# Optimization experiments

Hardware: AMD Instinct MI355X
Metric: run time of the kernel (lower is better)

Reference implementation:

```python
import jax, jax.numpy as jnp
import numpy as np
import math

NH, NKV, HD = 8, 1, 128
SOFTCAP = 30.0
ROPE_BASE = 500000.0


def _rope_tables(T, hd, base):
    half = hd // 2
    inv_freq = 1.0 / (base ** (np.arange(half, dtype=np.float32) / half))
    t = np.arange(T, dtype=np.float32)
    ang = np.outer(t, inv_freq)  # [T, half]
    return jnp.asarray(np.cos(ang)), jnp.asarray(np.sin(ang))


def apply_rope(x, cos, sin):
    # x: [B, T, H, hd]; cos/sin: [T, hd//2]
    half = x.shape[-1] // 2
    x1, x2 = x[..., :half], x[..., half:]
    T = x.shape[1]
    c = cos[:T][None, :, None, :]
    s = sin[:T][None, :, None, :]
    return jnp.concatenate([x1 * c - x2 * s, x1 * s + x2 * c], axis=-1)


def setup_inputs() -> dict:
    key = jax.random.key(0)
    ks = jax.random.split(key, 5)
    B, T, D = 4, 2048, 1024
    KD = NKV * HD
    x = jax.random.normal(ks[0], (B, T, D), dtype=jnp.float32)
    Wq = jax.random.normal(ks[1], (D, D), dtype=jnp.float32) * (D ** -0.5)
    Wk = jax.random.normal(ks[2], (KD, D), dtype=jnp.float32) * (D ** -0.5)
    Wv = jax.random.normal(ks[3], (KD, D), dtype=jnp.float32) * (D ** -0.5)
    Wo = jax.random.normal(ks[4], (D, D), dtype=jnp.float32) * (D ** -0.5)
    qk_gain = jnp.full((NH,), 1.5, dtype=jnp.float32)  # qk_gain_init
    cos, sin = _rope_tables(T, HD, ROPE_BASE)
    return {"x": x, "Wq": Wq, "Wk": Wk, "Wv": Wv, "Wo": Wo,
            "qk_gain": qk_gain, "cos": cos, "sin": sin}


def reference(x, Wq, Wk, Wv, Wo, qk_gain, cos, sin):
    B, T, D = x.shape
    # projections (QuantLinear with qat disabled == plain linear, no bias)
    q = (x @ Wq.T).reshape(B, T, NH, HD)
    k = (x @ Wk.T).reshape(B, T, NKV, HD)
    v = (x @ Wv.T).reshape(B, T, NKV, HD)
    q = apply_rope(q, cos, sin)
    k = apply_rope(k, cos, sin)
    # learned per-head QK gain applied to queries
    q = q * qk_gain[None, None, :, 1 - 1][..., None] if False else q * qk_gain[None, None, :, None]
    # GQA: broadcast the single kv head across NH query heads
    scale = 1.0 / math.sqrt(HD)
    scores = jnp.einsum('bqhd,bkgd->bhqk', q, k) * scale  # g==NKV==1 broadcast
    # logit softcap before masking/softmax
    scores = SOFTCAP * jnp.tanh(scores / SOFTCAP)
    causal = jnp.tril(jnp.ones((T, T), dtype=bool))
    scores = jnp.where(causal[None, None], scores, -jnp.inf)
    attn = jax.nn.softmax(scores, axis=-1)  # [B, NH, T, T]
    out = jnp.einsum('bhqk,bkgd->bqhd', attn, v).reshape(B, T, NH * HD)
    return out @ Wo.T
```

## Files before the change

### kernel.cpp

```cpp
#include <hip/hip_runtime.h>
#include <hip/hip_bf16.h>

#define B_ 4
#define T_ 2048
#define D_ 1024
#define NH_ 8
#define HD_ 128

typedef short short8 __attribute__((ext_vector_type(8)));
typedef float floatx4 __attribute__((ext_vector_type(4)));

#if __has_builtin(__builtin_amdgcn_exp2f)
#define EXP2F __builtin_amdgcn_exp2f
#else
#define EXP2F exp2f
#endif
#if __has_builtin(__builtin_amdgcn_rcpf)
#define RCPF __builtin_amdgcn_rcpf
#else
__device__ __forceinline__ float RCPF(float x) { return 1.f / x; }
#endif

#if __has_builtin(__builtin_amdgcn_global_load_lds)
#define G2L(gp, lp)                                                        \
  __builtin_amdgcn_global_load_lds(                                        \
      (const __attribute__((address_space(1))) unsigned int*)(gp),         \
      (__attribute__((address_space(3))) unsigned int*)(lp), 16, 0, 0)
#else
#define G2L(gp, lp) (*(uint4*)(lp) = *(const uint4*)(gp))
#endif

__device__ __forceinline__ unsigned short f2b(float f) {
  union { float fl; unsigned int i; } v; v.fl = f;
  unsigned int r = v.i + 0x7fffu + ((v.i >> 16) & 1u);
  return (unsigned short)(r >> 16);
}
__device__ __forceinline__ unsigned int pack_bf16(float a, float b) {
  unsigned int ua = __float_as_uint(a) + 0x8000u;
  unsigned int ub = __float_as_uint(b) + 0x8000u;
  return (ua >> 16) | (ub & 0xffff0000u);
}

__global__ __launch_bounds__(256) void cvt_kernel(
    const float* __restrict__ x,  const float* __restrict__ wq,
    const float* __restrict__ wk, const float* __restrict__ wv,
    const float* __restrict__ wo, unsigned short* __restrict__ dst)
{
  size_t i = ((size_t)blockIdx.x * 256 + threadIdx.x) * 8;
  const float* src; size_t off;
  if      (i <  8388608u) { src = x;  off = i; }
  else if (i <  9437184u) { src = wq; off = i - 8388608u; }
  else if (i <  9568256u) { src = wk; off = i - 9437184u; }
  else if (i <  9699328u) { src = wv; off = i - 9568256u; }
  else                    { src = wo; off = i - 9699328u; }
  float4 a = *(const float4*)(src + off);
  float4 b = *(const float4*)(src + off + 4);
  uint4 o;
  o.x = pack_bf16(a.x, a.y); o.y = pack_bf16(a.z, a.w);
  o.z = pack_bf16(b.x, b.y); o.w = pack_bf16(b.z, b.w);
  *(uint4*)(dst + i) = o;
}

template <bool C_F32>
__device__ __forceinline__ void gemm_body_1024(
    const unsigned short* __restrict__ Arow0,
    const unsigned short* __restrict__ Btile,
    void* __restrict__ Cb, int ldC)
{
  __shared__ unsigned short As[128 * 32];
  __shared__ unsigned short Bs[128 * 32];
  const int tid = threadIdx.x;
  const int lane = tid & 63;
  const int w = tid >> 6;
  const int wr = w >> 1, wc = w & 1;
  const int l15 = lane & 15, quad = lane >> 4;

  const unsigned short* a_src = Arow0 + (size_t)(tid >> 2) * 1024 + (tid & 3) * 8;
  const unsigned short* b_src = Btile + (size_t)(tid >> 2) * 1024 + (tid & 3) * 8;
  unsigned short* a_dst = &As[(tid >> 2) * 32 + (tid & 3) * 8];
  unsigned short* b_dst = &Bs[(tid >> 2) * 32 + (tid & 3) * 8];

  floatx4 zero = {0.f, 0.f, 0.f, 0.f};
  floatx4 acc[4][4];
#pragma unroll
  for (int i = 0; i < 4; i++)
#pragma unroll
    for (int j = 0; j < 4; j++) acc[i][j] = zero;

  for (int k0 = 0; k0 < 1024; k0 += 32) {
    __syncthreads();
    G2L(a_src + k0,         a_dst);
    G2L(a_src + 65536 + k0, a_dst + 2048);
    G2L(b_src + k0,         b_dst);
    G2L(b_src + 65536 + k0, b_dst + 2048);
    __syncthreads();
    short8 af[4], bfr[4];
#pragma unroll
    for (int i = 0; i < 4; i++)
      af[i] = *(const short8*)&As[(wr * 64 + i * 16 + l15) * 32 + quad * 8];
#pragma unroll
    for (int j = 0; j < 4; j++)
      bfr[j] = *(const short8*)&Bs[(wc * 64 + j * 16 + l15) * 32 + quad * 8];
#pragma unroll
    for (int i = 0; i < 4; i++)
#pragma unroll
      for (int j = 0; j < 4; j++)
        acc[i][j] = __builtin_amdgcn_mfma_f32_16x16x32_bf16(af[i], bfr[j], acc[i][j], 0, 0, 0);
  }
#pragma unroll
  for (int i = 0; i < 4; i++)
#pragma unroll
    for (int j = 0; j < 4; j++)
#pragma unroll
      for (int r = 0; r < 4; r++) {
        size_t off = (size_t)(wr * 64 + i * 16 + quad * 4 + r) * ldC + wc * 64 + j * 16 + l15;
        if (C_F32) ((float*)Cb)[off] = acc[i][j][r];
        else ((unsigned short*)Cb)[off] = f2b(acc[i][j][r]);
      }
}

__global__ __launch_bounds__(256) void gemm_qkv_kernel(
    const unsigned short* __restrict__ x,
    const unsigned short* __restrict__ Wq,
    const unsigned short* __restrict__ Wk,
    const unsigned short* __restrict__ Wv,
    unsigned short* __restrict__ q,
    unsigned short* __restrict__ k,
    unsigned short* __restrict__ v)
{
  const int bx = blockIdx.x, by = blockIdx.y;
  const unsigned short* Btile;
  unsigned short* C;
  int ldC, col0;
  if (by < 8) { Btile = Wq + (size_t)by * 128 * 1024; C = q; ldC = 1024; col0 = by * 128; }
  else if (by == 8) { Btile = Wk; C = k; ldC = 128; col0 = 0; }
  else { Btile = Wv; C = v; ldC = 128; col0 = 0; }
  gemm_body_1024<false>(x + (size_t)bx * 128 * 1024, Btile,
                        C + (size_t)bx * 128 * ldC + col0, ldC);
}

__global__ __launch_bounds__(256) void gemm_out_kernel(
    const unsigned short* __restrict__ ao,
    const unsigned short* __restrict__ Wo,
    float* __restrict__ out)
{
  const int bx = blockIdx.x, by = blockIdx.y;
  gemm_body_1024<true>(ao + (size_t)bx * 128 * 1024, Wo + (size_t)by * 128 * 1024,
                       out + (size_t)bx * 128 * 1024 + by * 128, 1024);
}

__global__ __launch_bounds__(256) void rope_kernel(
    unsigned short* __restrict__ q,
    unsigned short* __restrict__ k,
    const float* __restrict__ cosT,
    const float* __restrict__ sinT,
    const float* __restrict__ gain)
{
  const int NQ = B_ * T_ * NH_ * 64;
  int idx = blockIdx.x * 256 + threadIdx.x;
  if (idx < NQ) {
    int i = idx & 63, h = (idx >> 6) & 7, bt = idx >> 9, t = bt & (T_ - 1);
    float c = cosT[t * 64 + i], s = sinT[t * 64 + i];
    float g = gain[h] * 0.0029462782549439484f;
    size_t base = (size_t)bt * 1024 + h * 128;
    float x1 = __bfloat162float(*(const __hip_bfloat16*)&q[base + i]);
    float x2 = __bfloat162float(*(const __hip_bfloat16*)&q[base + 64 + i]);
    q[base + i]      = f2b((x1 * c - x2 * s) * g);
    q[base + 64 + i] = f2b((x1 * s + x2 * c) * g);
  } else if (idx < NQ + B_ * T_ * 64) {
    int j = idx - NQ;
    int i = j & 63, bt = j >> 6, t = bt & (T_ - 1);
    float c = cosT[t * 64 + i], s = sinT[t * 64 + i];
    size_t base = (size_t)bt * 128;
    float x1 = __bfloat162float(*(const __hip_bfloat16*)&k[base + i]);
    float x2 = __bfloat162float(*(const __hip_bfloat16*)&k[base + 64 + i]);
    k[base + i]      = f2b(x1 * c - x2 * s);
    k[base + 64 + i] = f2b(x1 * s + x2 * c);
  }
}

__global__ __launch_bounds__(256) void vtrans_kernel(
    const unsigned short* __restrict__ v,
    unsigned short* __restrict__ vT)
{
  __shared__ unsigned short tile[32 * 136];
  const int b = blockIdx.y, t0 = blockIdx.x * 32, tid = threadIdx.x;
  for (int u = tid; u < 512; u += 256) {
    int r = u >> 4, c = u & 15;
    *(uint4*)&tile[r * 136 + c * 8] =
        *(const uint4*)(v + ((size_t)(b * T_ + t0 + r)) * 128 + c * 8);
  }
  __syncthreads();
  for (int u = tid; u < 512; u += 256) {
    int d = u >> 2, c = u & 3;
    short8 val;
#pragma unroll
    for (int j = 0; j < 8; j++) val[j] = (short)tile[(c * 8 + j) * 136 + d];
    *(short8*)(vT + ((size_t)(b * 128 + d)) * T_ + t0 + c * 8) = val;
  }
}

__global__ __launch_bounds__(256) void attn_kernel(
    const unsigned short* __restrict__ q,
    const unsigned short* __restrict__ k,
    const unsigned short* __restrict__ vT,
    unsigned short* __restrict__ ao)
{
  __shared__ unsigned short Ks[16 * 264];
  __shared__ unsigned short Vts[128 * 40];
  __shared__ unsigned short Pw[4][32 * 40];

  const int pr = blockIdx.x, h = blockIdx.y, b = blockIdx.z;
  const int tid = threadIdx.x, lane = tid & 63, w = tid >> 6;
  const int l15 = lane & 15, quad = lane >> 4;

  const unsigned short* ksrc =
      k + (size_t)b * T_ * 128 + (size_t)(tid >> 4) * 128 + (tid & 15) * 8;
  unsigned short* kdst0 = &Ks[(tid & 15) * 264 + (tid >> 4) * 8];
  unsigned short* kdst1 = kdst0 + 16 * 8;
  const unsigned short* vsrc =
      vT + (size_t)b * 128 * T_ + (size_t)(tid >> 2) * T_ + (tid & 3) * 8;
  unsigned short* vdst0 = &Vts[(tid >> 2) * 40 + (tid & 3) * 8];
  unsigned short* vdst1 = vdst0 + 64 * 40;

  const floatx4 zero = {0.f, 0.f, 0.f, 0.f};

  for (int pass = 0; pass < 2; pass++) {
    const int qblock = pass ? (15 - pr) : pr;
    const int qbase = qblock * 128;
    const int qw = qbase + w * 32;
    const int nkt = qblock * 4 + 4;

    short8 qf[2][4];
#pragma unroll
    for (int g = 0; g < 2; g++) {
      const unsigned short* qrow =
          q + ((size_t)(b * T_ + qw + g * 16 + l15) * NH_ + h) * HD_;
#pragma unroll
      for (int c = 0; c < 4; c++) qf[g][c] = *(const short8*)(qrow + c * 32 + quad * 8);
    }

    float l_i[2] = {0.f, 0.f};
    floatx4 acc[8][2];
#pragma unroll
    for (int d = 0; d < 8; d++) { acc[d][0] = zero; acc[d][1] = zero; }

    uint4 kr0 = *(const uint4*)(ksrc);
    uint4 kr1 = *(const uint4*)(ksrc + 2048);
    uint4 vr0 = *(const uint4*)(vsrc);
    uint4 vr1 = *(const uint4*)(vsrc + (size_t)64 * T_);

    for (int kt = 0; kt < nkt; kt++) {
      __syncthreads();
      *(uint4*)kdst0 = kr0; *(uint4*)kdst1 = kr1;
      *(uint4*)vdst0 = vr0; *(uint4*)vdst1 = vr1;
      int ktn = (kt + 1 < nkt) ? kt + 1 : kt;
      kr0 = *(const uint4*)(ksrc + (size_t)ktn * 4096);
      kr1 = *(const uint4*)(ksrc + (size_t)ktn * 4096 + 2048);
      vr0 = *(const uint4*)(vsrc + ktn * 32);
      vr1 = *(const uint4*)(vsrc + (size_t)64 * T_ + ktn * 32);
      __syncthreads();

      if (kt * 32 <= qw + 31) {
        floatx4 st[2][2] = {{zero, zero}, {zero, zero}};
#pragma unroll
        for (int c = 0; c < 4; c++) {
          const int dg = (c * 4 + quad) * 264;
          short8 kf0 = *(const short8*)&Ks[dg + l15 * 8];
          short8 kf1 = *(const short8*)&Ks[dg + (16 + l15) * 8];
          st[0][0] = __builtin_amdgcn_mfma_f32_16x16x32_bf16(kf0, qf[0][c], st[0][0], 0, 0, 0);
          st[0][1] = __builtin_amdgcn_mfma_f32_16x16x32_bf16(kf0, qf[1][c], st[0][1], 0, 0, 0);
          st[1][0] = __builtin_amdgcn_mfma_f32_16x16x32_bf16(kf1, qf[0][c], st[1][0], 0, 0, 0);
          st[1][1] = __builtin_amdgcn_mfma_f32_16x16x32_bf16(kf1, qf[1][c], st[1][1], 0, 0, 0);
        }
        float rs[2] = {0.f, 0.f};
#pragma unroll
        for (int f = 0; f < 2; f++)
#pragma unroll
          for (int g = 0; g < 2; g++) {
            float pv[4];
            const int qrow = qw + g * 16 + l15;
#pragma unroll
            for (int r = 0; r < 4; r++) {
              float s = st[f][g][r];
              float e = EXP2F(2.8853901f * s);
              float u = RCPF(e + 1.f);
              float p = EXP2F(-86.561707f * u);
              int key = kt * 32 + f * 16 + quad * 4 + r;
              p = (key <= qrow) ? p : 0.f;
              pv[r] = p;
              rs[g] += p;
            }
            uint2 pk;
            pk.x = pack_bf16(pv[0], pv[1]);
            pk.y = pack_bf16(pv[2], pv[3]);
            *(uint2*)&Pw[w][(g * 16 + l15) * 40 + f * 16 + quad * 4] = pk;
          }
#pragma unroll
        for (int g = 0; g < 2; g++) {
          float r2 = rs[g] + __shfl_xor(rs[g], 16);
          l_i[g] += r2 + __shfl_xor(r2, 32);
        }
        asm volatile("s_waitcnt lgkmcnt(0)" ::: "memory");
        short8 pf0 = *(const short8*)&Pw[w][l15 * 40 + quad * 8];
        short8 pf1 = *(const short8*)&Pw[w][(16 + l15) * 40 + quad * 8];
#pragma unroll
        for (int d = 0; d < 8; d++) {
          short8 vf = *(const short8*)&Vts[(d * 16 + l15) * 40 + quad * 8];
          acc[d][0] = __builtin_amdgcn_mfma_f32_16x16x32_bf16(vf, pf0, acc[d][0], 0, 0, 0);
          acc[d][1] = __builtin_amdgcn_mfma_f32_16x16x32_bf16(vf, pf1, acc[d][1], 0, 0, 0);
        }
      }
    }

#pragma unroll
    for (int g = 0; g < 2; g++) {
      float linv = 1.f / l_i[g];
      unsigned short* aop =
          ao + ((size_t)(b * T_ + qw + g * 16 + l15) * NH_ + h) * HD_ + quad * 4;
#pragma unroll
      for (int d = 0; d < 8; d++) {
        uint2 o;
        o.x = pack_bf16(acc[d][g][0] * linv, acc[d][g][1] * linv);
        o.y = pack_bf16(acc[d][g][2] * linv, acc[d][g][3] * linv);
        *(uint2*)(aop + d * 16) = o;
      }
    }
  }
}

extern "C" void kernel_launch(void* const* d_in, const int* in_sizes, int n_in,
                              void* d_out, int out_size, void* d_ws, size_t ws_size,
                              hipStream_t stream) {
  const float* x    = (const float*)d_in[0];
  const float* Wq   = (const float*)d_in[1];
  const float* Wk   = (const float*)d_in[2];
  const float* Wv   = (const float*)d_in[3];
  const float* Wo   = (const float*)d_in[4];
  const float* gain = (const float*)d_in[5];
  const float* cosT = (const float*)d_in[6];
  const float* sinT = (const float*)d_in[7];
  float* out = (float*)d_out;

  unsigned short* ws = (unsigned short*)d_ws;
  unsigned short* blob = ws;
  unsigned short* xb  = blob;
  unsigned short* Wqb = blob + 8388608u;
  unsigned short* Wkb = blob + 9437184u;
  unsigned short* Wvb = blob + 9568256u;
  unsigned short* Wob = blob + 9699328u;
  unsigned short* q   = ws + 10747904u;
  unsigned short* kk  = ws + 19136512u;
  unsigned short* v   = ws + 20185088u;
  unsigned short* vT  = ws + 21233664u;
  unsigned short* ao  = xb;

  cvt_kernel<<<5248, 256, 0, stream>>>(x, Wq, Wk, Wv, Wo, blob);
  gemm_qkv_kernel<<<dim3(64, 10), 256, 0, stream>>>(xb, Wqb, Wkb, Wvb, q, kk, v);
  rope_kernel<<<18432, 256, 0, stream>>>(q, kk, cosT, sinT, gain);
  vtrans_kernel<<<dim3(64, 4), 256, 0, stream>>>(v, vT);
  attn_kernel<<<dim3(8, 8, 4), 256, 0, stream>>>(q, kk, vT, ao);
  gemm_out_kernel<<<dim3(64, 8), 256, 0, stream>>>(ao, Wob, out);
}
```

Baseline: 262.2 us.

## Split attention key range across two blocks and combine partial results

```diff
diff --git a/kernel.cpp b/kernel.cpp
--- a/kernel.cpp
+++ b/kernel.cpp
@@ -40,6 +40,8 @@
   unsigned int ub = __float_as_uint(b) + 0x8000u;
   return (ua >> 16) | (ub & 0xffff0000u);
 }
+__device__ __forceinline__ float blo(unsigned int u) { return __uint_as_float(u << 16); }
+__device__ __forceinline__ float bhi(unsigned int u) { return __uint_as_float(u & 0xffff0000u); }
 
 __global__ __launch_bounds__(256) void cvt_kernel(
     const float* __restrict__ x,  const float* __restrict__ wq,
@@ -200,17 +202,23 @@
   }
 }
 
+template <int SPLIT>
 __global__ __launch_bounds__(256) void attn_kernel(
     const unsigned short* __restrict__ q,
     const unsigned short* __restrict__ k,
     const unsigned short* __restrict__ vT,
-    unsigned short* __restrict__ ao)
+    unsigned short* __restrict__ ao,
+    unsigned short* __restrict__ O0,
+    float* __restrict__ l0,
+    float* __restrict__ l1)
 {
   __shared__ unsigned short Ks[16 * 264];
   __shared__ unsigned short Vts[128 * 40];
   __shared__ unsigned short Pw[4][32 * 40];
 
-  const int pr = blockIdx.x, h = blockIdx.y, b = blockIdx.z;
+  const int h = blockIdx.y, b = blockIdx.z;
+  const int pr   = SPLIT ? (blockIdx.x >> 1) : blockIdx.x;
+  const int half = SPLIT ? (blockIdx.x & 1) : 0;
   const int tid = threadIdx.x, lane = tid & 63, w = tid >> 6;
   const int l15 = lane & 15, quad = lane >> 4;
 
@@ -229,7 +237,15 @@
     const int qblock = pass ? (15 - pr) : pr;
     const int qbase = qblock * 128;
     const int qw = qbase + w * 32;
-    const int nkt = qblock * 4 + 4;
+    int ktBeg, ktEnd;
+    if (SPLIT) {
+      int hn = 2 * qblock + 2;
+      ktBeg = half ? hn : 0;
+      ktEnd = half ? 2 * hn : hn;
+    } else {
+      ktBeg = 0;
+      ktEnd = 4 * qblock + 4;
+    }
 
     short8 qf[2][4];
 #pragma unroll
@@ -245,16 +261,16 @@
 #pragma unroll
     for (int d = 0; d < 8; d++) { acc[d][0] = zero; acc[d][1] = zero; }
 
-    uint4 kr0 = *(const uint4*)(ksrc);
-    uint4 kr1 = *(const uint4*)(ksrc + 2048);
-    uint4 vr0 = *(const uint4*)(vsrc);
-    uint4 vr1 = *(const uint4*)(vsrc + (size_t)64 * T_);
-
-    for (int kt = 0; kt < nkt; kt++) {
+    uint4 kr0 = *(const uint4*)(ksrc + (size_t)ktBeg * 4096);
+    uint4 kr1 = *(const uint4*)(ksrc + (size_t)ktBeg * 4096 + 2048);
+    uint4 vr0 = *(const uint4*)(vsrc + ktBeg * 32);
+    uint4 vr1 = *(const uint4*)(vsrc + (size_t)64 * T_ + ktBeg * 32);
+
+    for (int kt = ktBeg; kt < ktEnd; kt++) {
       __syncthreads();
       *(uint4*)kdst0 = kr0; *(uint4*)kdst1 = kr1;
       *(uint4*)vdst0 = vr0; *(uint4*)vdst1 = vr1;
-      int ktn = (kt + 1 < nkt) ? kt + 1 : kt;
+      int ktn = (kt + 1 < ktEnd) ? kt + 1 : kt;
       kr0 = *(const uint4*)(ksrc + (size_t)ktn * 4096);
       kr1 = *(const uint4*)(ksrc + (size_t)ktn * 4096 + 2048);
       vr0 = *(const uint4*)(vsrc + ktn * 32);
@@ -315,18 +331,49 @@
 
 #pragma unroll
     for (int g = 0; g < 2; g++) {
-      float linv = 1.f / l_i[g];
-      unsigned short* aop =
-          ao + ((size_t)(b * T_ + qw + g * 16 + l15) * NH_ + h) * HD_ + quad * 4;
-#pragma unroll
-      for (int d = 0; d < 8; d++) {
-        uint2 o;
-        o.x = pack_bf16(acc[d][g][0] * linv, acc[d][g][1] * linv);
-        o.y = pack_bf16(acc[d][g][2] * linv, acc[d][g][3] * linv);
-        *(uint2*)(aop + d * 16) = o;
+      const size_t rowidx = (size_t)(b * T_ + qw + g * 16 + l15) * NH_ + h;
+      if (!SPLIT) {
+        float linv = 1.f / l_i[g];
+        unsigned short* aop = ao + rowidx * HD_ + quad * 4;
+#pragma unroll
+        for (int d = 0; d < 8; d++) {
+          uint2 o;
+          o.x = pack_bf16(acc[d][g][0] * linv, acc[d][g][1] * linv);
+          o.y = pack_bf16(acc[d][g][2] * linv, acc[d][g][3] * linv);
+          *(uint2*)(aop + d * 16) = o;
+        }
+      } else {
+        unsigned short* dst = (half ? ao : O0) + rowidx * HD_ + quad * 4;
+#pragma unroll
+        for (int d = 0; d < 8; d++) {
+          uint2 o;
+          o.x = pack_bf16(acc[d][g][0], acc[d][g][1]);
+          o.y = pack_bf16(acc[d][g][2], acc[d][g][3]);
+          *(uint2*)(dst + d * 16) = o;
+        }
+        if (quad == 0) (half ? l1 : l0)[rowidx] = l_i[g];
       }
     }
   }
+}
+
+__global__ __launch_bounds__(256) void combine_kernel(
+    const unsigned short* __restrict__ O0,
+    const float* __restrict__ l0,
+    const float* __restrict__ l1,
+    unsigned short* __restrict__ ao)
+{
+  size_t i = ((size_t)blockIdx.x * 256 + threadIdx.x) * 8;
+  size_t r = i >> 7;
+  float linv = RCPF(l0[r] + l1[r]);
+  uint4 a = *(const uint4*)(O0 + i);
+  uint4 c = *(const uint4*)(ao + i);
+  uint4 o;
+  o.x = pack_bf16((blo(a.x) + blo(c.x)) * linv, (bhi(a.x) + bhi(c.x)) * linv);
+  o.y = pack_bf16((blo(a.y) + blo(c.y)) * linv, (bhi(a.y) + bhi(c.y)) * linv);
+  o.z = pack_bf16((blo(a.z) + blo(c.z)) * linv, (bhi(a.z) + bhi(c.z)) * linv);
+  o.w = pack_bf16((blo(a.w) + blo(c.w)) * linv, (bhi(a.w) + bhi(c.w)) * linv);
+  *(uint4*)(ao + i) = o;
 }
 
 extern "C" void kernel_launch(void* const* d_in, const int* in_sizes, int n_in,
@@ -354,11 +401,20 @@
   unsigned short* v   = ws + 20185088u;
   unsigned short* vT  = ws + 21233664u;
   unsigned short* ao  = xb;
+  unsigned short* O0 = ws + 22282240u;
+  float* l0 = (float*)((char*)d_ws + 61341696u);
+  float* l1 = (float*)((char*)d_ws + 61603840u);
+  const bool split = ws_size >= 61865984ull;
 
   cvt_kernel<<<5248, 256, 0, stream>>>(x, Wq, Wk, Wv, Wo, blob);
   gemm_qkv_kernel<<<dim3(64, 10), 256, 0, stream>>>(xb, Wqb, Wkb, Wvb, q, kk, v);
   rope_kernel<<<18432, 256, 0, stream>>>(q, kk, cosT, sinT, gain);
   vtrans_kernel<<<dim3(64, 4), 256, 0, stream>>>(v, vT);
-  attn_kernel<<<dim3(8, 8, 4), 256, 0, stream>>>(q, kk, vT, ao);
+  if (split) {
+    attn_kernel<1><<<dim3(16, 8, 4), 256, 0, stream>>>(q, kk, vT, ao, O0, l0, l1);
+    combine_kernel<<<4096, 256, 0, stream>>>(O0, l0, l1, ao);
+  } else {
+    attn_kernel<0><<<dim3(8, 8, 4), 256, 0, stream>>>(q, kk, vT, ao, O0, l0, l1);
+  }
   gemm_out_kernel<<<dim3(64, 8), 256, 0, stream>>>(ao, Wob, out);
 }
```

After: 246.3 us. 1.06x faster.
